# Kernel optimization log

Hardware: AMD Instinct MI355X
Metric: run time of the kernel (lower is better)

The kernel has to match this reference:

```python
import jax, jax.numpy as jnp
import numpy as np

TOP_K = 200          # max detections kept per class (SSD Detect default)
CONF_THRESH = 0.01   # confidence threshold
NMS_THRESH = 0.45    # IoU threshold for greedy NMS
VAR0, VAR1 = 0.1, 0.2  # SSD prior-box variances


def setup_inputs() -> dict:
    key = jax.random.key(0)
    k1, k2, k3, k4 = jax.random.split(key, 4)
    B, A, C = 32, 24564, 21
    class_preds = jax.random.normal(k1, (B, A, C), jnp.float32)
    loc_preds = jax.random.normal(k2, (B, A, 4), jnp.float32) * 0.5
    # anchors in (cx, cy, w, h) form, values in [0, 1]
    cxcy = jax.random.uniform(k3, (A, 2), jnp.float32)
    wh = jax.random.uniform(k4, (A, 2), jnp.float32, minval=0.05, maxval=0.5)
    anchors = jnp.concatenate([cxcy, wh], axis=-1)
    return {"class_preds": class_preds, "loc_preds": loc_preds, "anchors": anchors}


def _decode(loc, anchors):
    # loc: [B, A, 4], anchors: [A, 4] (cx, cy, w, h) -> boxes [B, A, 4] (x1, y1, x2, y2)
    cxcy = anchors[:, :2] + loc[..., :2] * VAR0 * anchors[:, 2:]
    wh = anchors[:, 2:] * jnp.exp(loc[..., 2:] * VAR1)
    return jnp.concatenate([cxcy - wh * 0.5, cxcy + wh * 0.5], axis=-1)


def _pairwise_iou(boxes):
    # boxes: [K, 4] -> [K, K]
    area = jnp.prod(jnp.clip(boxes[:, 2:] - boxes[:, :2], 0.0), axis=-1)
    lt = jnp.maximum(boxes[:, None, :2], boxes[None, :, :2])
    rb = jnp.minimum(boxes[:, None, 2:], boxes[None, :, 2:])
    inter = jnp.prod(jnp.clip(rb - lt, 0.0), axis=-1)
    return inter / (area[:, None] + area[None, :] - inter + 1e-9)


def _nms_one_class(scores_c, boxes_b):
    # scores_c: [A], boxes_b: [A, 4] -> [TOP_K, 5] (score, x1, y1, x2, y2)
    scores_m = jnp.where(scores_c > CONF_THRESH, scores_c, 0.0)
    top_s, idx = jax.lax.top_k(scores_m, TOP_K)
    top_b = boxes_b[idx]                      # [TOP_K, 4]
    ious = _pairwise_iou(top_b)               # [TOP_K, TOP_K]
    rng = jnp.arange(TOP_K)

    def body(i, keep):
        sup = (ious[i] > NMS_THRESH) & (rng > i) & keep[i]
        return keep & ~sup

    keep = jax.lax.fori_loop(0, TOP_K, body, jnp.ones((TOP_K,), bool))
    keep = keep & (top_s > 0.0)
    kf = keep.astype(top_s.dtype)
    return jnp.concatenate([(top_s * kf)[:, None], top_b * kf[:, None]], axis=-1)


def reference(class_preds, loc_preds, anchors):
    B, A, C = class_preds.shape
    conf = jax.nn.softmax(class_preds, axis=-1)          # [B, A, C]
    boxes = _decode(loc_preds, anchors)                  # [B, A, 4]
    scores = jnp.swapaxes(conf[..., 1:], 1, 2)           # [B, C-1, A] (skip background)
    per_image = jax.vmap(_nms_one_class, in_axes=(0, None))   # over classes
    out = jax.vmap(per_image, in_axes=(0, 0))(scores, boxes)  # [B, C-1, TOP_K, 5]
    bg = jnp.zeros((B, 1, TOP_K, 5), out.dtype)          # background row stays empty
    return jnp.concatenate([bg, out], axis=1)            # [B, C, TOP_K, 5]
```

## Files before the change

### kernel.cpp

```cpp
#include <hip/hip_runtime.h>
#include <math.h>


constexpr int CNUM  = 21;
constexpr int CC    = 20;
constexpr int TOPK  = 200;
constexpr int NT    = 256;
constexpr int NBINS = 1024;
constexpr int SLICES = 8;
constexpr int SEGCAP = 256;
constexpr int CAP   = SLICES * SEGCAP;
constexpr unsigned BIN_BASE = 0x3C23u;

__device__ __forceinline__ float cr_expf(float x) {
  return (float)exp((double)x);
}

__global__ __launch_bounds__(256) void softmax_T4(
    const float* __restrict__ cls, float* __restrict__ sw, int B, int A) {
  const long long r0 = ((long long)blockIdx.x * 256 + threadIdx.x) * 4;
  const long long BA = (long long)B * A;
  if (r0 >= BA) return;

  if (r0 + 3 < BA && (A & 3) == 0) {
    const int b = (int)(r0 / A);
    const int a0 = (int)(r0 - (long long)b * A);
    float xf[84];
    const float4* p = (const float4*)(cls + r0 * CNUM);
#pragma unroll
    for (int k = 0; k < 21; ++k) {
      float4 q = p[k];
      xf[4 * k + 0] = q.x; xf[4 * k + 1] = q.y;
      xf[4 * k + 2] = q.z; xf[4 * k + 3] = q.w;
    }
    float S[4];
#pragma unroll
    for (int r = 0; r < 4; ++r) {
      const int base = 21 * r;
      float m = xf[base];
#pragma unroll
      for (int c = 1; c < CNUM; ++c) m = fmaxf(m, xf[base + c]);
      float s = 0.f;
#pragma unroll
      for (int c = 0; c < CNUM; ++c) {
        float e = cr_expf(__fsub_rn(xf[base + c], m));
        xf[base + c] = e;
        s = __fadd_rn(s, e);
      }
      S[r] = s;
    }
#pragma unroll
    for (int c = 1; c < CNUM; ++c) {
      float4 w;
      w.x = __fdiv_rn(xf[0 * 21 + c], S[0]);
      w.y = __fdiv_rn(xf[1 * 21 + c], S[1]);
      w.z = __fdiv_rn(xf[2 * 21 + c], S[2]);
      w.w = __fdiv_rn(xf[3 * 21 + c], S[3]);
      *(float4*)(sw + ((size_t)b * CC + (c - 1)) * A + a0) = w;
    }
  } else {
    for (long long r = r0; r < BA && r < r0 + 4; ++r) {
      const int b = (int)(r / A);
      const int a = (int)(r - (long long)b * A);
      const float* row = cls + r * CNUM;
      float x[CNUM];
#pragma unroll
      for (int c = 0; c < CNUM; ++c) x[c] = row[c];
      float m = x[0];
#pragma unroll
      for (int c = 1; c < CNUM; ++c) m = fmaxf(m, x[c]);
      float e[CNUM], s = 0.f;
#pragma unroll
      for (int c = 0; c < CNUM; ++c) {
        e[c] = cr_expf(__fsub_rn(x[c], m));
        s = __fadd_rn(s, e[c]);
      }
#pragma unroll
      for (int c = 1; c < CNUM; ++c)
        sw[((size_t)b * CC + (c - 1)) * A + a] = __fdiv_rn(e[c], s);
    }
  }
}

__global__ __launch_bounds__(256) void hist_k(
    const float* __restrict__ sw, unsigned* __restrict__ ghist, int A) {
  __shared__ unsigned hist[NBINS];
  const int bc = blockIdx.x / SLICES;
  const int sl = blockIdx.x % SLICES;
  const int tid = threadIdx.x;
  for (int i = tid; i < NBINS; i += NT) hist[i] = 0;
  __syncthreads();

  const float* srow = sw + (size_t)bc * A;
  const int n4 = A >> 2;
  const int per4 = (n4 + SLICES - 1) / SLICES;
  const int s4 = sl * per4, e4 = min(n4, s4 + per4);
  const float4* srow4 = (const float4*)srow;
  for (int i = s4 + tid; i < e4; i += NT) {
    float4 v = srow4[i];
    float vs[4] = {v.x, v.y, v.z, v.w};
#pragma unroll
    for (int j = 0; j < 4; ++j) {
      float s = vs[j];
      if (s > 0.01f) {
        unsigned bits = __float_as_uint(s);
        int bin = (int)(bits >> 16) - (int)BIN_BASE;
        bin = bin < (NBINS - 1) ? bin : (NBINS - 1);
        atomicAdd(&hist[bin], 1u);
      }
    }
  }
  if (sl == 0)
    for (int a = (n4 << 2) + tid; a < A; a += NT) {
      float s = srow[a];
      if (s > 0.01f) {
        unsigned bits = __float_as_uint(s);
        int bin = (int)(bits >> 16) - (int)BIN_BASE;
        bin = bin < (NBINS - 1) ? bin : (NBINS - 1);
        atomicAdd(&hist[bin], 1u);
      }
    }
  __syncthreads();
  for (int i = tid; i < NBINS; i += NT) {
    unsigned h = hist[i];
    if (h) atomicAdd(&ghist[(size_t)bc * NBINS + i], h);
  }
}

__global__ __launch_bounds__(64) void thr_k(
    const unsigned* __restrict__ ghist, unsigned* __restrict__ thr) {
  __shared__ unsigned binsh[NBINS];
  __shared__ unsigned ps[64];
  const int bc = blockIdx.x;
  const int lane = threadIdx.x;
  unsigned sum = 0;
#pragma unroll
  for (int k = 0; k < NBINS / 64; ++k) {
    int b = lane * (NBINS / 64) + k;
    unsigned h = ghist[(size_t)bc * NBINS + b];
    binsh[b] = h;
    sum += h;
  }
  ps[lane] = sum;
  __syncthreads();
  if (lane == 0) {
    unsigned cum = 0;
    int T = 0;
    for (int l = 63; l >= 0; --l) {
      if (cum + ps[l] >= (unsigned)TOPK) {
        for (int b = l * (NBINS / 64) + (NBINS / 64) - 1; b >= l * (NBINS / 64); --b) {
          cum += binsh[b];
          if (cum >= (unsigned)TOPK) { T = b; break; }
        }
        break;
      }
      cum += ps[l];
    }
    thr[bc] = (unsigned)T + BIN_BASE;
  }
}

__global__ __launch_bounds__(256) void collect_k(
    const float* __restrict__ sw, const unsigned* __restrict__ thr,
    unsigned long long* __restrict__ cand, unsigned* __restrict__ cnt8, int A) {
  __shared__ unsigned s_pos;
  __shared__ unsigned long long s_keys[SEGCAP];
  const int bc = blockIdx.x / SLICES;
  const int sl = blockIdx.x % SLICES;
  const int tid = threadIdx.x;
  if (tid == 0) s_pos = 0u;
  __syncthreads();

  const unsigned thr_hi = thr[bc];
  const float* srow = sw + (size_t)bc * A;
  const int n4 = A >> 2;
  const int per4 = (n4 + SLICES - 1) / SLICES;
  const int s4 = sl * per4, e4 = min(n4, s4 + per4);
  const float4* srow4 = (const float4*)srow;
  for (int i = s4 + tid; i < e4; i += NT) {
    float4 v = srow4[i];
    float vs[4] = {v.x, v.y, v.z, v.w};
#pragma unroll
    for (int j = 0; j < 4; ++j) {
      float s = vs[j];
      if (s > 0.01f) {
        unsigned bits = __float_as_uint(s);
        if ((bits >> 16) >= thr_hi) {
          unsigned a = (unsigned)(i * 4 + j);
          unsigned p = atomicAdd(&s_pos, 1u);
          if (p < SEGCAP)
            s_keys[p] = ((unsigned long long)bits << 32) | (unsigned)(~a);
        }
      }
    }
  }
  if (sl == 0)
    for (int a = (n4 << 2) + tid; a < A; a += NT) {
      float s = srow[a];
      if (s > 0.01f) {
        unsigned bits = __float_as_uint(s);
        if ((bits >> 16) >= thr_hi) {
          unsigned p = atomicAdd(&s_pos, 1u);
          if (p < SEGCAP)
            s_keys[p] = ((unsigned long long)bits << 32) | (unsigned)(~(unsigned)a);
        }
      }
    }
  __syncthreads();
  const unsigned cnt = s_pos < (unsigned)SEGCAP ? s_pos : (unsigned)SEGCAP;
  unsigned long long* cbase = cand + ((size_t)bc * SLICES + sl) * SEGCAP;
  for (unsigned i = tid; i < cnt; i += NT) cbase[i] = s_keys[i];
  if (tid == 0) cnt8[bc * SLICES + sl] = cnt;
}

__global__ __launch_bounds__(256) void nms_k(
    const unsigned long long* __restrict__ cand, const unsigned* __restrict__ cnt8,
    const float* __restrict__ loc, const float* __restrict__ anch,
    float* __restrict__ out, int B, int A) {
  __shared__ unsigned long long keys[CAP];
  __shared__ float bxv[TOPK][4];
  __shared__ float barea[TOPK];
  __shared__ float bscore[TOPK];
  __shared__ unsigned sup[TOPK][8];
  __shared__ unsigned keepm[8];
  __shared__ int s_segcnt[SLICES];
  __shared__ int s_segoff[SLICES + 1];

  const int tid = threadIdx.x;
  const int bc = blockIdx.x;
  const int b = bc / CNUM;
  const int c = bc - b * CNUM;
  float* obase = out + (size_t)bc * (TOPK * 5);
  if (c == 0) {
    for (int i = tid; i < TOPK * 5; i += NT) obase[i] = 0.f;
    return;
  }
  const int bc20 = b * CC + (c - 1);

  if (tid < SLICES) {
    unsigned v = cnt8[bc20 * SLICES + tid];
    s_segcnt[tid] = v < (unsigned)SEGCAP ? (int)v : SEGCAP;
  }
  __syncthreads();
  if (tid == 0) {
    int o = 0;
    for (int s2 = 0; s2 < SLICES; ++s2) { s_segoff[s2] = o; o += s_segcnt[s2]; }
    s_segoff[SLICES] = o;
  }
  __syncthreads();
  const int n_cand = s_segoff[SLICES];

  int P2 = 256;
  while (P2 < n_cand) P2 <<= 1;

  const unsigned long long* cb = cand + (size_t)bc20 * SLICES * SEGCAP;
  for (int s2 = 0; s2 < SLICES; ++s2)
    for (int i = tid; i < s_segcnt[s2]; i += NT)
      keys[s_segoff[s2] + i] = cb[s2 * SEGCAP + i];
  for (int i = tid; i < P2; i += NT)
    if (i >= n_cand) keys[i] = 0ull;
  __syncthreads();

  for (int size = 2; size <= P2; size <<= 1) {
    for (int stride = size >> 1; stride > 0; stride >>= 1) {
      for (int i = tid; i < P2; i += NT) {
        int j = i ^ stride;
        if (j > i) {
          unsigned long long ki = keys[i], kj = keys[j];
          bool desc = ((i & size) == 0);
          if (desc ? (ki < kj) : (ki > kj)) { keys[i] = kj; keys[j] = ki; }
        }
      }
      __syncthreads();
    }
  }

  const int n = n_cand < TOPK ? n_cand : TOPK;

  if (tid < n) {
    unsigned long long k = keys[tid];
    float s = __uint_as_float((unsigned)(k >> 32));
    unsigned a = ~(unsigned)(k & 0xFFFFFFFFull);
    const float* lp = loc + ((size_t)b * A + a) * 4;
    const float* an = anch + (size_t)a * 4;
    float l0 = lp[0], l1 = lp[1], l2 = lp[2], l3 = lp[3];
    float acx = an[0], acy = an[1], aw = an[2], ah = an[3];
    float cx = __fadd_rn(acx, __fmul_rn(__fmul_rn(l0, 0.1f), aw));
    float cy = __fadd_rn(acy, __fmul_rn(__fmul_rn(l1, 0.1f), ah));
    float w  = __fmul_rn(aw, cr_expf(__fmul_rn(l2, 0.2f)));
    float h  = __fmul_rn(ah, cr_expf(__fmul_rn(l3, 0.2f)));
    float hw = __fmul_rn(w, 0.5f), hh = __fmul_rn(h, 0.5f);
    float x1 = __fsub_rn(cx, hw), y1 = __fsub_rn(cy, hh);
    float x2 = __fadd_rn(cx, hw), y2 = __fadd_rn(cy, hh);
    bxv[tid][0] = x1; bxv[tid][1] = y1; bxv[tid][2] = x2; bxv[tid][3] = y2;
    barea[tid] = __fmul_rn(fmaxf(__fsub_rn(x2, x1), 0.f),
                           fmaxf(__fsub_rn(y2, y1), 0.f));
    bscore[tid] = s;
  }
  for (int i = tid; i < TOPK * 8; i += NT) ((unsigned*)sup)[i] = 0u;
  __syncthreads();

  for (int idx = tid; idx < TOPK * TOPK; idx += NT) {
    int i = idx / TOPK;
    int j = idx - i * TOPK;
    if (j > i && j < n && i < n) {
      float ltx = fmaxf(bxv[i][0], bxv[j][0]);
      float lty = fmaxf(bxv[i][1], bxv[j][1]);
      float rbx = fminf(bxv[i][2], bxv[j][2]);
      float rby = fminf(bxv[i][3], bxv[j][3]);
      float iw = fmaxf(__fsub_rn(rbx, ltx), 0.f);
      float ih = fmaxf(__fsub_rn(rby, lty), 0.f);
      float inter = __fmul_rn(iw, ih);
      float denom = __fadd_rn(__fsub_rn(__fadd_rn(barea[i], barea[j]), inter), 1e-9f);
      float iou = __fdiv_rn(inter, denom);
      if (iou > 0.45f) atomicOr(&sup[i][j >> 5], 1u << (j & 31));
    }
  }
  __syncthreads();

  if (tid == 0) {
    unsigned km[8];
#pragma unroll
    for (int w = 0; w < 8; ++w) {
      int lo = w * 32;
      unsigned m2;
      if (n >= lo + 32) m2 = 0xFFFFFFFFu;
      else if (n <= lo) m2 = 0u;
      else m2 = (1u << (n - lo)) - 1u;
      km[w] = m2;
    }
    for (int i = 0; i < n; ++i) {
      if ((km[i >> 5] >> (i & 31)) & 1u) {
#pragma unroll
        for (int w = 0; w < 8; ++w) km[w] &= ~sup[i][w];
      }
    }
#pragma unroll
    for (int w = 0; w < 8; ++w) keepm[w] = km[w];
  }
  __syncthreads();

  if (tid < TOPK) {
    float s = 0.f, o0 = 0.f, o1 = 0.f, o2 = 0.f, o3 = 0.f;
    if (tid < n && ((keepm[tid >> 5] >> (tid & 31)) & 1u)) {
      s = bscore[tid];
      o0 = bxv[tid][0]; o1 = bxv[tid][1]; o2 = bxv[tid][2]; o3 = bxv[tid][3];
    }
    obase[tid * 5 + 0] = s;
    obase[tid * 5 + 1] = o0;
    obase[tid * 5 + 2] = o1;
    obase[tid * 5 + 3] = o2;
    obase[tid * 5 + 4] = o3;
  }
}

__global__ __launch_bounds__(256) void softmax_MS(
    const float* __restrict__ cls, float2* __restrict__ ms, int B, int A) {
  int i = blockIdx.x * 256 + threadIdx.x;
  if (i >= B * A) return;
  const float* row = cls + (size_t)i * CNUM;
  float x[CNUM];
#pragma unroll
  for (int c = 0; c < CNUM; ++c) x[c] = row[c];
  float m = x[0];
#pragma unroll
  for (int c = 1; c < CNUM; ++c) m = fmaxf(m, x[c]);
  float S = 0.f;
#pragma unroll
  for (int c = 0; c < CNUM; ++c) S = __fadd_rn(S, cr_expf(__fsub_rn(x[c], m)));
  ms[i] = make_float2(m, S);
}

__device__ __forceinline__ float score_direct(const float* __restrict__ cls,
                                              int b, int A, int a, int c) {
  const float* row = cls + ((size_t)b * A + a) * CNUM;
  float x[CNUM];
#pragma unroll
  for (int k = 0; k < CNUM; ++k) x[k] = row[k];
  float m = x[0];
#pragma unroll
  for (int k = 1; k < CNUM; ++k) m = fmaxf(m, x[k]);
  float S = 0.f, ec = 0.f;
#pragma unroll
  for (int k = 0; k < CNUM; ++k) {
    float e = cr_expf(__fsub_rn(x[k], m));
    S = __fadd_rn(S, e);
    if (k == c) ec = e;
  }
  return __fdiv_rn(ec, S);
}

template <int MODE>
__global__ __launch_bounds__(256) void topk_nms(
    const float* __restrict__ cls, const float* __restrict__ sw,
    const float* __restrict__ loc, const float* __restrict__ anch,
    float* __restrict__ out, int B, int A) {
  __shared__ unsigned hist[NBINS];
  __shared__ unsigned long long keys[CAP];
  __shared__ float bxv[TOPK][4];
  __shared__ float barea[TOPK];
  __shared__ float bscore[TOPK];
  __shared__ unsigned sup[TOPK][8];
  __shared__ unsigned keepm[8];
  __shared__ int s_cnt;
  __shared__ int s_T;

  const int tid = threadIdx.x;
  const int bc = blockIdx.x;
  const int b = bc / CNUM;
  const int c = bc - b * CNUM;
  float* obase = out + (size_t)bc * (TOPK * 5);
  if (c == 0) {
    for (int i = tid; i < TOPK * 5; i += NT) obase[i] = 0.f;
    return;
  }
  const float* srow =
      (MODE == 0) ? (sw + ((size_t)b * CC + (c - 1)) * A) : nullptr;
  const float2* msrow = (MODE == 2) ? ((const float2*)sw + (size_t)b * A) : nullptr;

  auto get_score = [&](int a) -> float {
    if (MODE == 0) return srow[a];
    if (MODE == 2) {
      float2 v = msrow[a];
      float xc = cls[((size_t)b * A + a) * CNUM + c];
      return __fdiv_rn(cr_expf(__fsub_rn(xc, v.x)), v.y);
    }
    return score_direct(cls, b, A, a, c);
  };

  for (int i = tid; i < NBINS; i += NT) hist[i] = 0;
  if (tid == 0) { s_cnt = 0; s_T = 0; }
  __syncthreads();

  for (int a = tid; a < A; a += NT) {
    float s = get_score(a);
    if (s > 0.01f) {
      unsigned bits = __float_as_uint(s);
      int bin = (int)(bits >> 16) - (int)BIN_BASE;
      bin = bin < (NBINS - 1) ? bin : (NBINS - 1);
      atomicAdd(&hist[bin], 1u);
    }
  }
  __syncthreads();

  if (tid == 0) {
    unsigned cum = 0;
    int T = 0;
    for (int i = NBINS - 1; i >= 0; --i) {
      cum += hist[i];
      if (cum >= TOPK) { T = i; break; }
    }
    s_T = T;
  }
  __syncthreads();
  const unsigned thr_hi = (unsigned)s_T + BIN_BASE;

  for (int a = tid; a < A; a += NT) {
    float s = get_score(a);
    if (s > 0.01f) {
      unsigned bits = __float_as_uint(s);
      if ((bits >> 16) >= thr_hi) {
        int pos = atomicAdd(&s_cnt, 1);
        if (pos < CAP)
          keys[pos] = ((unsigned long long)bits << 32) | (unsigned)(~(unsigned)a);
      }
    }
  }
  __syncthreads();
  int cnt = s_cnt < CAP ? s_cnt : CAP;
  for (int i = tid; i < CAP; i += NT)
    if (i >= cnt) keys[i] = 0ull;
  __syncthreads();

  for (int size = 2; size <= CAP; size <<= 1) {
    for (int stride = size >> 1; stride > 0; stride >>= 1) {
      for (int i = tid; i < CAP; i += NT) {
        int j = i ^ stride;
        if (j > i) {
          unsigned long long ki = keys[i], kj = keys[j];
          bool desc = ((i & size) == 0);
          if (desc ? (ki < kj) : (ki > kj)) { keys[i] = kj; keys[j] = ki; }
        }
      }
      __syncthreads();
    }
  }

  const int n = cnt < TOPK ? cnt : TOPK;

  if (tid < n) {
    unsigned long long k = keys[tid];
    float s = __uint_as_float((unsigned)(k >> 32));
    unsigned a = ~(unsigned)(k & 0xFFFFFFFFull);
    const float* lp = loc + ((size_t)b * A + a) * 4;
    const float* an = anch + (size_t)a * 4;
    float l0 = lp[0], l1 = lp[1], l2 = lp[2], l3 = lp[3];
    float acx = an[0], acy = an[1], aw = an[2], ah = an[3];
    float cx = __fadd_rn(acx, __fmul_rn(__fmul_rn(l0, 0.1f), aw));
    float cy = __fadd_rn(acy, __fmul_rn(__fmul_rn(l1, 0.1f), ah));
    float w  = __fmul_rn(aw, cr_expf(__fmul_rn(l2, 0.2f)));
    float h  = __fmul_rn(ah, cr_expf(__fmul_rn(l3, 0.2f)));
    float hw = __fmul_rn(w, 0.5f), hh = __fmul_rn(h, 0.5f);
    float x1 = __fsub_rn(cx, hw), y1 = __fsub_rn(cy, hh);
    float x2 = __fadd_rn(cx, hw), y2 = __fadd_rn(cy, hh);
    bxv[tid][0] = x1; bxv[tid][1] = y1; bxv[tid][2] = x2; bxv[tid][3] = y2;
    barea[tid] = __fmul_rn(fmaxf(__fsub_rn(x2, x1), 0.f),
                           fmaxf(__fsub_rn(y2, y1), 0.f));
    bscore[tid] = s;
  }
  for (int i = tid; i < TOPK * 8; i += NT) ((unsigned*)sup)[i] = 0u;
  __syncthreads();

  for (int idx = tid; idx < TOPK * TOPK; idx += NT) {
    int i = idx / TOPK;
    int j = idx - i * TOPK;
    if (j > i && j < n && i < n) {
      float ltx = fmaxf(bxv[i][0], bxv[j][0]);
      float lty = fmaxf(bxv[i][1], bxv[j][1]);
      float rbx = fminf(bxv[i][2], bxv[j][2]);
      float rby = fminf(bxv[i][3], bxv[j][3]);
      float iw = fmaxf(__fsub_rn(rbx, ltx), 0.f);
      float ih = fmaxf(__fsub_rn(rby, lty), 0.f);
      float inter = __fmul_rn(iw, ih);
      float denom = __fadd_rn(__fsub_rn(__fadd_rn(barea[i], barea[j]), inter), 1e-9f);
      float iou = __fdiv_rn(inter, denom);
      if (iou > 0.45f) atomicOr(&sup[i][j >> 5], 1u << (j & 31));
    }
  }
  __syncthreads();

  if (tid == 0) {
    unsigned km[8];
#pragma unroll
    for (int w = 0; w < 8; ++w) {
      int lo = w * 32;
      unsigned m2;
      if (n >= lo + 32) m2 = 0xFFFFFFFFu;
      else if (n <= lo) m2 = 0u;
      else m2 = (1u << (n - lo)) - 1u;
      km[w] = m2;
    }
    for (int i = 0; i < n; ++i) {
      if ((km[i >> 5] >> (i & 31)) & 1u) {
#pragma unroll
        for (int w = 0; w < 8; ++w) km[w] &= ~sup[i][w];
      }
    }
#pragma unroll
    for (int w = 0; w < 8; ++w) keepm[w] = km[w];
  }
  __syncthreads();

  if (tid < TOPK) {
    float s = 0.f, o0 = 0.f, o1 = 0.f, o2 = 0.f, o3 = 0.f;
    if (tid < n && ((keepm[tid >> 5] >> (tid & 31)) & 1u)) {
      s = bscore[tid];
      o0 = bxv[tid][0]; o1 = bxv[tid][1]; o2 = bxv[tid][2]; o3 = bxv[tid][3];
    }
    obase[tid * 5 + 0] = s;
    obase[tid * 5 + 1] = o0;
    obase[tid * 5 + 2] = o1;
    obase[tid * 5 + 3] = o2;
    obase[tid * 5 + 4] = o3;
  }
}

extern "C" void kernel_launch(void* const* d_in, const int* in_sizes, int n_in,
                              void* d_out, int out_size, void* d_ws, size_t ws_size,
                              hipStream_t stream) {
  const float* cls  = (const float*)d_in[0];
  const float* loc  = (const float*)d_in[1];
  const float* anch = (const float*)d_in[2];
  float* out = (float*)d_out;

  const int A = in_sizes[2] / 4;
  const int B = in_sizes[1] / (4 * A);
  const long long BA = (long long)B * A;
  const int NBC = B * CC;

  auto al = [](size_t x) { return (x + 255) & ~(size_t)255; };
  const size_t sz_sw   = al((size_t)NBC * A * sizeof(float));
  const size_t sz_cand = al((size_t)NBC * SLICES * SEGCAP * sizeof(unsigned long long));
  const size_t sz_hist = al((size_t)NBC * NBINS * sizeof(unsigned));
  const size_t sz_cnt  = al((size_t)NBC * SLICES * sizeof(unsigned));
  const size_t sz_thr  = al((size_t)NBC * sizeof(unsigned));
  const size_t need_new = sz_sw + sz_cand + sz_hist + sz_cnt + sz_thr;

  if (ws_size >= need_new) {
    char* w = (char*)d_ws;
    float* sw = (float*)w;
    unsigned long long* cand = (unsigned long long*)(w + sz_sw);
    unsigned* ghist = (unsigned*)(w + sz_sw + sz_cand);
    unsigned* cnt8 = (unsigned*)(w + sz_sw + sz_cand + sz_hist);
    unsigned* thr = (unsigned*)(w + sz_sw + sz_cand + sz_hist + sz_cnt);

    hipMemsetAsync(ghist, 0, sz_hist, stream);

    const int k1_grid = (int)((BA / 4 + 255) / 256) + 1;
    softmax_T4<<<k1_grid, 256, 0, stream>>>(cls, sw, B, A);
    hist_k<<<NBC * SLICES, NT, 0, stream>>>(sw, ghist, A);
    thr_k<<<NBC, 64, 0, stream>>>(ghist, thr);
    collect_k<<<NBC * SLICES, NT, 0, stream>>>(sw, thr, cand, cnt8, A);
    nms_k<<<B * CNUM, NT, 0, stream>>>(cand, cnt8, loc, anch, out, B, A);
    return;
  }

  const size_t need_full = (size_t)NBC * A * sizeof(float);
  const size_t need_ms   = (size_t)BA * sizeof(float2);
  const int tot = (int)BA;
  if (ws_size >= need_full) {
    float* sw = (float*)d_ws;
    const int k1_grid = (int)((BA / 4 + 255) / 256) + 1;
    softmax_T4<<<k1_grid, 256, 0, stream>>>(cls, sw, B, A);
    topk_nms<0><<<B * CNUM, NT, 0, stream>>>(cls, sw, loc, anch, out, B, A);
  } else if (ws_size >= need_ms) {
    float2* ms = (float2*)d_ws;
    softmax_MS<<<(tot + 255) / 256, 256, 0, stream>>>(cls, ms, B, A);
    topk_nms<2><<<B * CNUM, NT, 0, stream>>>(cls, (const float*)ms, loc, anch, out, B, A);
  } else {
    topk_nms<1><<<B * CNUM, NT, 0, stream>>>(cls, nullptr, loc, anch, out, B, A);
  }
}
```

Before: 232.7 us.

## Replace full IoU matrix plus serial scan with sequential per-row greedy NMS

In nms_k, the pairwise IoU bitmask build (40k pairs with atomicOr) and the single-thread serial keep scan are replaced. Now each thread owns one candidate box in registers and loops over i. It checks suppression only against boxes still kept, with a block barrier per iteration. This skips IoU work for already-suppressed rows and removes the serial thread-0 loop, at the cost of up to 200 __syncthreads per block. The other kernels are only moved in the file, not changed.

```diff
diff --git a/kernel.cpp b/kernel.cpp
--- a/kernel.cpp
+++ b/kernel.cpp
@@ -218,11 +218,9 @@
     const float* __restrict__ loc, const float* __restrict__ anch,
     float* __restrict__ out, int B, int A) {
   __shared__ unsigned long long keys[CAP];
-  __shared__ float bxv[TOPK][4];
+  __shared__ float4 bxv[TOPK];
   __shared__ float barea[TOPK];
-  __shared__ float bscore[TOPK];
-  __shared__ unsigned sup[TOPK][8];
-  __shared__ unsigned keepm[8];
+  __shared__ unsigned keep[TOPK];
   __shared__ int s_segcnt[SLICES];
   __shared__ int s_segoff[SLICES + 1];
 
@@ -276,6 +274,197 @@
   }
 
   const int n = n_cand < TOPK ? n_cand : TOPK;
+
+  float mx1 = 0.f, my1 = 0.f, mx2 = 0.f, my2 = 0.f, marea = 0.f, mscore = 0.f;
+  if (tid < TOPK) keep[tid] = (tid < n) ? 1u : 0u;
+  if (tid < n) {
+    unsigned long long k = keys[tid];
+    mscore = __uint_as_float((unsigned)(k >> 32));
+    unsigned a = ~(unsigned)(k & 0xFFFFFFFFull);
+    const float* lp = loc + ((size_t)b * A + a) * 4;
+    const float* an = anch + (size_t)a * 4;
+    float l0 = lp[0], l1 = lp[1], l2 = lp[2], l3 = lp[3];
+    float acx = an[0], acy = an[1], aw = an[2], ah = an[3];
+    float cx = __fadd_rn(acx, __fmul_rn(__fmul_rn(l0, 0.1f), aw));
+    float cy = __fadd_rn(acy, __fmul_rn(__fmul_rn(l1, 0.1f), ah));
+    float w  = __fmul_rn(aw, cr_expf(__fmul_rn(l2, 0.2f)));
+    float h  = __fmul_rn(ah, cr_expf(__fmul_rn(l3, 0.2f)));
+    float hw = __fmul_rn(w, 0.5f), hh = __fmul_rn(h, 0.5f);
+    mx1 = __fsub_rn(cx, hw); my1 = __fsub_rn(cy, hh);
+    mx2 = __fadd_rn(cx, hw); my2 = __fadd_rn(cy, hh);
+    marea = __fmul_rn(fmaxf(__fsub_rn(mx2, mx1), 0.f),
+                      fmaxf(__fsub_rn(my2, my1), 0.f));
+    bxv[tid] = make_float4(mx1, my1, mx2, my2);
+    barea[tid] = marea;
+  }
+  __syncthreads();
+
+  unsigned my_keep = (tid < n) ? 1u : 0u;
+  for (int i = 0; i < n; ++i) {
+    unsigned ki = keep[i];
+    float4 bi = bxv[i];
+    float ia = barea[i];
+    if (ki && my_keep && tid > i && tid < n) {
+      float ltx = fmaxf(bi.x, mx1);
+      float lty = fmaxf(bi.y, my1);
+      float rbx = fminf(bi.z, mx2);
+      float rby = fminf(bi.w, my2);
+      float iw = fmaxf(__fsub_rn(rbx, ltx), 0.f);
+      float ih = fmaxf(__fsub_rn(rby, lty), 0.f);
+      float inter = __fmul_rn(iw, ih);
+      float denom = __fadd_rn(__fsub_rn(__fadd_rn(ia, marea), inter), 1e-9f);
+      float iou = __fdiv_rn(inter, denom);
+      if (iou > 0.45f) { my_keep = 0u; keep[tid] = 0u; }
+    }
+    __syncthreads();
+  }
+
+  if (tid < TOPK) {
+    float s = 0.f, o0 = 0.f, o1 = 0.f, o2 = 0.f, o3 = 0.f;
+    if (tid < n && my_keep) {
+      s = mscore; o0 = mx1; o1 = my1; o2 = mx2; o3 = my2;
+    }
+    obase[tid * 5 + 0] = s;
+    obase[tid * 5 + 1] = o0;
+    obase[tid * 5 + 2] = o1;
+    obase[tid * 5 + 3] = o2;
+    obase[tid * 5 + 4] = o3;
+  }
+}
+
+__global__ __launch_bounds__(256) void softmax_MS(
+    const float* __restrict__ cls, float2* __restrict__ ms, int B, int A) {
+  int i = blockIdx.x * 256 + threadIdx.x;
+  if (i >= B * A) return;
+  const float* row = cls + (size_t)i * CNUM;
+  float x[CNUM];
+#pragma unroll
+  for (int c = 0; c < CNUM; ++c) x[c] = row[c];
+  float m = x[0];
+#pragma unroll
+  for (int c = 1; c < CNUM; ++c) m = fmaxf(m, x[c]);
+  float S = 0.f;
+#pragma unroll
+  for (int c = 0; c < CNUM; ++c) S = __fadd_rn(S, cr_expf(__fsub_rn(x[c], m)));
+  ms[i] = make_float2(m, S);
+}
+
+__device__ __forceinline__ float score_direct(const float* __restrict__ cls,
+                                              int b, int A, int a, int c) {
+  const float* row = cls + ((size_t)b * A + a) * CNUM;
+  float x[CNUM];
+#pragma unroll
+  for (int k = 0; k < CNUM; ++k) x[k] = row[k];
+  float m = x[0];
+#pragma unroll
+  for (int k = 1; k < CNUM; ++k) m = fmaxf(m, x[k]);
+  float S = 0.f, ec = 0.f;
+#pragma unroll
+  for (int k = 0; k < CNUM; ++k) {
+    float e = cr_expf(__fsub_rn(x[k], m));
+    S = __fadd_rn(S, e);
+    if (k == c) ec = e;
+  }
+  return __fdiv_rn(ec, S);
+}
+
+template <int MODE>
+__global__ __launch_bounds__(256) void topk_nms(
+    const float* __restrict__ cls, const float* __restrict__ sw,
+    const float* __restrict__ loc, const float* __restrict__ anch,
+    float* __restrict__ out, int B, int A) {
+  __shared__ unsigned hist[NBINS];
+  __shared__ unsigned long long keys[CAP];
+  __shared__ float bxv[TOPK][4];
+  __shared__ float barea[TOPK];
+  __shared__ float bscore[TOPK];
+  __shared__ unsigned sup[TOPK][8];
+  __shared__ unsigned keepm[8];
+  __shared__ int s_cnt;
+  __shared__ int s_T;
+
+  const int tid = threadIdx.x;
+  const int bc = blockIdx.x;
+  const int b = bc / CNUM;
+  const int c = bc - b * CNUM;
+  float* obase = out + (size_t)bc * (TOPK * 5);
+  if (c == 0) {
+    for (int i = tid; i < TOPK * 5; i += NT) obase[i] = 0.f;
+    return;
+  }
+  const float* srow =
+      (MODE == 0) ? (sw + ((size_t)b * CC + (c - 1)) * A) : nullptr;
+  const float2* msrow = (MODE == 2) ? ((const float2*)sw + (size_t)b * A) : nullptr;
+
+  auto get_score = [&](int a) -> float {
+    if (MODE == 0) return srow[a];
+    if (MODE == 2) {
+      float2 v = msrow[a];
+      float xc = cls[((size_t)b * A + a) * CNUM + c];
+      return __fdiv_rn(cr_expf(__fsub_rn(xc, v.x)), v.y);
+    }
+    return score_direct(cls, b, A, a, c);
+  };
+
+  for (int i = tid; i < NBINS; i += NT) hist[i] = 0;
+  if (tid == 0) { s_cnt = 0; s_T = 0; }
+  __syncthreads();
+
+  for (int a = tid; a < A; a += NT) {
+    float s = get_score(a);
+    if (s > 0.01f) {
+      unsigned bits = __float_as_uint(s);
+      int bin = (int)(bits >> 16) - (int)BIN_BASE;
+      bin = bin < (NBINS - 1) ? bin : (NBINS - 1);
+      atomicAdd(&hist[bin], 1u);
+    }
+  }
+  __syncthreads();
+
+  if (tid == 0) {
+    unsigned cum = 0;
+    int T = 0;
+    for (int i = NBINS - 1; i >= 0; --i) {
+      cum += hist[i];
+      if (cum >= TOPK) { T = i; break; }
+    }
+    s_T = T;
+  }
+  __syncthreads();
+  const unsigned thr_hi = (unsigned)s_T + BIN_BASE;
+
+  for (int a = tid; a < A; a += NT) {
+    float s = get_score(a);
+    if (s > 0.01f) {
+      unsigned bits = __float_as_uint(s);
+      if ((bits >> 16) >= thr_hi) {
+        int pos = atomicAdd(&s_cnt, 1);
+        if (pos < CAP)
+          keys[pos] = ((unsigned long long)bits << 32) | (unsigned)(~(unsigned)a);
+      }
+    }
+  }
+  __syncthreads();
+  int cnt = s_cnt < CAP ? s_cnt : CAP;
+  for (int i = tid; i < CAP; i += NT)
+    if (i >= cnt) keys[i] = 0ull;
+  __syncthreads();
+
+  for (int size = 2; size <= CAP; size <<= 1) {
+    for (int stride = size >> 1; stride > 0; stride >>= 1) {
+      for (int i = tid; i < CAP; i += NT) {
+        int j = i ^ stride;
+        if (j > i) {
+          unsigned long long ki = keys[i], kj = keys[j];
+          bool desc = ((i & size) == 0);
+          if (desc ? (ki < kj) : (ki > kj)) { keys[i] = kj; keys[j] = ki; }
+        }
+      }
+      __syncthreads();
+    }
+  }
+
+  const int n = cnt < TOPK ? cnt : TOPK;
 
   if (tid < n) {
     unsigned long long k = keys[tid];
@@ -354,217 +543,6 @@
   }
 }
 
-__global__ __launch_bounds__(256) void softmax_MS(
-    const float* __restrict__ cls, float2* __restrict__ ms, int B, int A) {
-  int i = blockIdx.x * 256 + threadIdx.x;
-  if (i >= B * A) return;
-  const float* row = cls + (size_t)i * CNUM;
-  float x[CNUM];
-#pragma unroll
-  for (int c = 0; c < CNUM; ++c) x[c] = row[c];
-  float m = x[0];
-#pragma unroll
-  for (int c = 1; c < CNUM; ++c) m = fmaxf(m, x[c]);
-  float S = 0.f;
-#pragma unroll
-  for (int c = 0; c < CNUM; ++c) S = __fadd_rn(S, cr_expf(__fsub_rn(x[c], m)));
-  ms[i] = make_float2(m, S);
-}
-
-__device__ __forceinline__ float score_direct(const float* __restrict__ cls,
-                                              int b, int A, int a, int c) {
-  const float* row = cls + ((size_t)b * A + a) * CNUM;
-  float x[CNUM];
-#pragma unroll
-  for (int k = 0; k < CNUM; ++k) x[k] = row[k];
-  float m = x[0];
-#pragma unroll
-  for (int k = 1; k < CNUM; ++k) m = fmaxf(m, x[k]);
-  float S = 0.f, ec = 0.f;
-#pragma unroll
-  for (int k = 0; k < CNUM; ++k) {
-    float e = cr_expf(__fsub_rn(x[k], m));
-    S = __fadd_rn(S, e);
-    if (k == c) ec = e;
-  }
-  return __fdiv_rn(ec, S);
-}
-
-template <int MODE>
-__global__ __launch_bounds__(256) void topk_nms(
-    const float* __restrict__ cls, const float* __restrict__ sw,
-    const float* __restrict__ loc, const float* __restrict__ anch,
-    float* __restrict__ out, int B, int A) {
-  __shared__ unsigned hist[NBINS];
-  __shared__ unsigned long long keys[CAP];
-  __shared__ float bxv[TOPK][4];
-  __shared__ float barea[TOPK];
-  __shared__ float bscore[TOPK];
-  __shared__ unsigned sup[TOPK][8];
-  __shared__ unsigned keepm[8];
-  __shared__ int s_cnt;
-  __shared__ int s_T;
-
-  const int tid = threadIdx.x;
-  const int bc = blockIdx.x;
-  const int b = bc / CNUM;
-  const int c = bc - b * CNUM;
-  float* obase = out + (size_t)bc * (TOPK * 5);
-  if (c == 0) {
-    for (int i = tid; i < TOPK * 5; i += NT) obase[i] = 0.f;
-    return;
-  }
-  const float* srow =
-      (MODE == 0) ? (sw + ((size_t)b * CC + (c - 1)) * A) : nullptr;
-  const float2* msrow = (MODE == 2) ? ((const float2*)sw + (size_t)b * A) : nullptr;
-
-  auto get_score = [&](int a) -> float {
-    if (MODE == 0) return srow[a];
-    if (MODE == 2) {
-      float2 v = msrow[a];
-      float xc = cls[((size_t)b * A + a) * CNUM + c];
-      return __fdiv_rn(cr_expf(__fsub_rn(xc, v.x)), v.y);
-    }
-    return score_direct(cls, b, A, a, c);
-  };
-
-  for (int i = tid; i < NBINS; i += NT) hist[i] = 0;
-  if (tid == 0) { s_cnt = 0; s_T = 0; }
-  __syncthreads();
-
-  for (int a = tid; a < A; a += NT) {
-    float s = get_score(a);
-    if (s > 0.01f) {
-      unsigned bits = __float_as_uint(s);
-      int bin = (int)(bits >> 16) - (int)BIN_BASE;
-      bin = bin < (NBINS - 1) ? bin : (NBINS - 1);
-      atomicAdd(&hist[bin], 1u);
-    }
-  }
-  __syncthreads();
-
-  if (tid == 0) {
-    unsigned cum = 0;
-    int T = 0;
-    for (int i = NBINS - 1; i >= 0; --i) {
-      cum += hist[i];
-      if (cum >= TOPK) { T = i; break; }
-    }
-    s_T = T;
-  }
-  __syncthreads();
-  const unsigned thr_hi = (unsigned)s_T + BIN_BASE;
-
-  for (int a = tid; a < A; a += NT) {
-    float s = get_score(a);
-    if (s > 0.01f) {
-      unsigned bits = __float_as_uint(s);
-      if ((bits >> 16) >= thr_hi) {
-        int pos = atomicAdd(&s_cnt, 1);
-        if (pos < CAP)
-          keys[pos] = ((unsigned long long)bits << 32) | (unsigned)(~(unsigned)a);
-      }
-    }
-  }
-  __syncthreads();
-  int cnt = s_cnt < CAP ? s_cnt : CAP;
-  for (int i = tid; i < CAP; i += NT)
-    if (i >= cnt) keys[i] = 0ull;
-  __syncthreads();
-
-  for (int size = 2; size <= CAP; size <<= 1) {
-    for (int stride = size >> 1; stride > 0; stride >>= 1) {
-      for (int i = tid; i < CAP; i += NT) {
-        int j = i ^ stride;
-        if (j > i) {
-          unsigned long long ki = keys[i], kj = keys[j];
-          bool desc = ((i & size) == 0);
-          if (desc ? (ki < kj) : (ki > kj)) { keys[i] = kj; keys[j] = ki; }
-        }
-      }
-      __syncthreads();
-    }
-  }
-
-  const int n = cnt < TOPK ? cnt : TOPK;
-
-  if (tid < n) {
-    unsigned long long k = keys[tid];
-    float s = __uint_as_float((unsigned)(k >> 32));
-    unsigned a = ~(unsigned)(k & 0xFFFFFFFFull);
-    const float* lp = loc + ((size_t)b * A + a) * 4;
-    const float* an = anch + (size_t)a * 4;
-    float l0 = lp[0], l1 = lp[1], l2 = lp[2], l3 = lp[3];
-    float acx = an[0], acy = an[1], aw = an[2], ah = an[3];
-    float cx = __fadd_rn(acx, __fmul_rn(__fmul_rn(l0, 0.1f), aw));
-    float cy = __fadd_rn(acy, __fmul_rn(__fmul_rn(l1, 0.1f), ah));
-    float w  = __fmul_rn(aw, cr_expf(__fmul_rn(l2, 0.2f)));
-    float h  = __fmul_rn(ah, cr_expf(__fmul_rn(l3, 0.2f)));
-    float hw = __fmul_rn(w, 0.5f), hh = __fmul_rn(h, 0.5f);
-    float x1 = __fsub_rn(cx, hw), y1 = __fsub_rn(cy, hh);
-    float x2 = __fadd_rn(cx, hw), y2 = __fadd_rn(cy, hh);
-    bxv[tid][0] = x1; bxv[tid][1] = y1; bxv[tid][2] = x2; bxv[tid][3] = y2;
-    barea[tid] = __fmul_rn(fmaxf(__fsub_rn(x2, x1), 0.f),
-                           fmaxf(__fsub_rn(y2, y1), 0.f));
-    bscore[tid] = s;
-  }
-  for (int i = tid; i < TOPK * 8; i += NT) ((unsigned*)sup)[i] = 0u;
-  __syncthreads();
-
-  for (int idx = tid; idx < TOPK * TOPK; idx += NT) {
-    int i = idx / TOPK;
-    int j = idx - i * TOPK;
-    if (j > i && j < n && i < n) {
-      float ltx = fmaxf(bxv[i][0], bxv[j][0]);
-      float lty = fmaxf(bxv[i][1], bxv[j][1]);
-      float rbx = fminf(bxv[i][2], bxv[j][2]);
-      float rby = fminf(bxv[i][3], bxv[j][3]);
-      float iw = fmaxf(__fsub_rn(rbx, ltx), 0.f);
-      float ih = fmaxf(__fsub_rn(rby, lty), 0.f);
-      float inter = __fmul_rn(iw, ih);
-      float denom = __fadd_rn(__fsub_rn(__fadd_rn(barea[i], barea[j]), inter), 1e-9f);
-      float iou = __fdiv_rn(inter, denom);
-      if (iou > 0.45f) atomicOr(&sup[i][j >> 5], 1u << (j & 31));
-    }
-  }
-  __syncthreads();
-
-  if (tid == 0) {
-    unsigned km[8];
-#pragma unroll
-    for (int w = 0; w < 8; ++w) {
-      int lo = w * 32;
-      unsigned m2;
-      if (n >= lo + 32) m2 = 0xFFFFFFFFu;
-      else if (n <= lo) m2 = 0u;
-      else m2 = (1u << (n - lo)) - 1u;
-      km[w] = m2;
-    }
-    for (int i = 0; i < n; ++i) {
-      if ((km[i >> 5] >> (i & 31)) & 1u) {
-#pragma unroll
-        for (int w = 0; w < 8; ++w) km[w] &= ~sup[i][w];
-      }
-    }
-#pragma unroll
-    for (int w = 0; w < 8; ++w) keepm[w] = km[w];
-  }
-  __syncthreads();
-
-  if (tid < TOPK) {
-    float s = 0.f, o0 = 0.f, o1 = 0.f, o2 = 0.f, o3 = 0.f;
-    if (tid < n && ((keepm[tid >> 5] >> (tid & 31)) & 1u)) {
-      s = bscore[tid];
-      o0 = bxv[tid][0]; o1 = bxv[tid][1]; o2 = bxv[tid][2]; o3 = bxv[tid][3];
-    }
-    obase[tid * 5 + 0] = s;
-    obase[tid * 5 + 1] = o0;
-    obase[tid * 5 + 2] = o1;
-    obase[tid * 5 + 3] = o2;
-    obase[tid * 5 + 4] = o3;
-  }
-}
-
 extern "C" void kernel_launch(void* const* d_in, const int* in_sizes, int n_in,
                               void* d_out, int out_size, void* d_ws, size_t ws_size,
                               hipStream_t stream) {
```

Measured after the change: 217.2 us. 6.6% less time.
